# Kernel optimization log

Measured on AMD Instinct MI355X. Metric: run time of the kernel, lower is better.

## Reference

```python
import jax, jax.numpy as jnp
import numpy as np

B, N, M = 16, 2048, 2048


def setup_inputs() -> dict:
    key = jax.random.key(0)
    k1, k2, k3 = jax.random.split(key, 3)
    pred_dsmat = jax.random.uniform(k1, (B, N, M), dtype=jnp.float32)
    # valid sizes: src_ns <= tgt_ns so a permutation GT exists for every valid row
    src_ns = jax.random.randint(k2, (B,), 1024, 1537, dtype=jnp.int32)
    tgt_ns = jax.random.randint(k3, (B,), 1537, 2049, dtype=jnp.int32)
    # gt_perm: identity permutation restricted to the valid region (one 1 per valid row)
    i = jnp.arange(N)[:, None]
    j = jnp.arange(M)[None, :]
    eye = (i == j).astype(jnp.float32)  # [N, M]
    row_mask = (jnp.arange(N)[None, :] < src_ns[:, None]).astype(jnp.float32)  # [B, N]
    gt_perm = eye[None, :, :] * row_mask[:, :, None]  # [B, N, M]
    return {"pred_dsmat": pred_dsmat, "gt_perm": gt_perm,
            "src_ns": src_ns, "tgt_ns": tgt_ns, "beta_value": 0.1}


def reference(pred_dsmat, gt_perm, src_ns, tgt_ns, beta_value):
    Bn, Nn, Mn = pred_dsmat.shape
    row_mask = jnp.arange(Nn)[None, :] < src_ns[:, None]   # [B, N] bool
    col_mask = jnp.arange(Mn)[None, :] < tgt_ns[:, None]   # [B, M] bool
    mask = row_mask[:, :, None] & col_mask[:, None, :]     # [B, N, M]

    pred = jnp.clip(pred_dsmat, 0.0, 1.0) * mask
    gt = gt_perm * mask

    gt_pred = pred * gt                      # gt-selected predicted values
    row_gt = gt_pred.sum(axis=2)             # [B, N] per-row GT value
    col_gt = gt_pred.sum(axis=1)             # [B, M] per-col GT value
    row_cnt = gt.sum(axis=2)                 # [B, N] #GT matches per row
    col_cnt = gt.sum(axis=1)                 # [B, M] #GT matches per col

    # attention masks: entries >= (gt value - beta), restricted to valid region
    att_src = ((pred >= row_gt[:, :, None] - beta_value) & mask) * row_cnt[:, :, None]
    att_tgt = ((pred >= col_gt[:, None, :] - beta_value) & mask) * col_cnt[:, None, :]

    src_neg = jnp.sum(((att_src - gt) * pred) ** 2, axis=2)  # [B, N]
    src_pos = jnp.sum(gt_pred ** 2, axis=2)                  # [B, N]
    tgt_neg = jnp.sum(((att_tgt - gt) * pred) ** 2, axis=1)  # [B, M]

    # sum of tgt_neg over the GT-matched column of each row == dot with column counts
    corr = jnp.einsum('bm,bm->b', tgt_neg, col_cnt)          # [B]

    denom = 1.0 + src_neg + corr[:, None]                    # [B, N]
    num = jnp.where(row_mask, src_pos, 1.0)
    den = jnp.where(row_mask, denom, 1.0)
    loss = -0.5 * jnp.sum(jnp.log(num / den) * row_mask)
    n_sum = src_ns.sum().astype(pred.dtype)
    return loss / n_sum
```

## Files before the change

### kernel.cpp

```cpp
#include <hip/hip_runtime.h>

#define B_ 16
#define N_ 2048
#define M_ 2048
#define ROWS 64
#define WROWS 16

__device__ __forceinline__ float wave_sum(float v) {
#pragma unroll
    for (int off = 32; off >= 1; off >>= 1) v += __shfl_xor(v, off);
    return v;
}

extern "C" __global__ __launch_bounds__(256) void k_pass1(
    const float* __restrict__ pred, const float* __restrict__ gt,
    const int* __restrict__ src_ns, const int* __restrict__ tgt_ns,
    float* __restrict__ row_gt, float* __restrict__ row_cnt,
    float* __restrict__ col_gt, float* __restrict__ col_cnt)
{
    const int b = blockIdx.y;
    const int src = src_ns[b];
    const int band = blockIdx.x;
    if (band * ROWS >= src) return;
    const int tgt = tgt_ns[b];
    const int wave = threadIdx.x >> 6, lane = threadIdx.x & 63;
    const int base = b * (N_ * M_);

    float4 acg[8], accn[8];
#pragma unroll
    for (int j = 0; j < 8; ++j) { acg[j] = make_float4(0,0,0,0); accn[j] = make_float4(0,0,0,0); }

    const int row0 = band * ROWS + wave * WROWS;
    for (int r = 0; r < WROWS; ++r) {
        const int n = row0 + r;
        if (n >= src) break;
        const float4* prow = (const float4*)(pred + base + n * M_);
        const float4* grow = (const float4*)(gt + base + n * M_);
        float rg = 0.f, rc = 0.f;
#pragma unroll
        for (int j = 0; j < 8; ++j) {
            const int m4 = j * 64 + lane;
            const float4 p4 = prow[m4];
            const float4 g4 = grow[m4];
            const int mb = m4 * 4;
#define P1C(K, MB) do { \
    const bool ok = (mb + K) < tgt; \
    float p = fminf(fmaxf(p4.MB, 0.f), 1.f); p = ok ? p : 0.f; \
    const float g = ok ? g4.MB : 0.f; \
    const float gp = p * g; \
    rg += gp; rc += g; \
    acg[j].MB += gp; accn[j].MB += g; \
} while (0)
            P1C(0, x); P1C(1, y); P1C(2, z); P1C(3, w);
#undef P1C
        }
        rg = wave_sum(rg); rc = wave_sum(rc);
        if (lane == 0) { row_gt[b * N_ + n] = rg; row_cnt[b * N_ + n] = rc; }
    }

    __shared__ float4 s_cg[M_ / 4];
    __shared__ float4 s_cc[M_ / 4];
    for (int i = threadIdx.x; i < M_ / 4; i += 256) {
        s_cg[i] = make_float4(0,0,0,0);
        s_cc[i] = make_float4(0,0,0,0);
    }
    __syncthreads();
    for (int w = 0; w < 4; ++w) {
        if (wave == w) {
#pragma unroll
            for (int j = 0; j < 8; ++j) {
                const int i = j * 64 + lane;
                float4 v = s_cg[i];
                v.x += acg[j].x; v.y += acg[j].y; v.z += acg[j].z; v.w += acg[j].w;
                s_cg[i] = v;
                float4 u = s_cc[i];
                u.x += accn[j].x; u.y += accn[j].y; u.z += accn[j].z; u.w += accn[j].w;
                s_cc[i] = u;
            }
        }
        __syncthreads();
    }
    const float* fcg = (const float*)s_cg;
    const float* fcc = (const float*)s_cc;
    for (int i = threadIdx.x; i < M_; i += 256) {
        atomicAdd(&col_gt[b * M_ + i], fcg[i]);
        atomicAdd(&col_cnt[b * M_ + i], fcc[i]);
    }
}

extern "C" __global__ __launch_bounds__(256) void k_pass2(
    const float* __restrict__ pred, const float* __restrict__ gt,
    const int* __restrict__ src_ns, const int* __restrict__ tgt_ns,
    const float* __restrict__ beta_p,
    const float* __restrict__ row_gt, const float* __restrict__ row_cnt,
    const float* __restrict__ col_gt, const float* __restrict__ col_cnt,
    float* __restrict__ src_neg, float* __restrict__ src_pos,
    float* __restrict__ tgt_neg)
{
    const int b = blockIdx.y;
    const int src = src_ns[b];
    const int band = blockIdx.x;
    if (band * ROWS >= src) return;
    const int tgt = tgt_ns[b];
    const float beta = beta_p[0];
    const int wave = threadIdx.x >> 6, lane = threadIdx.x & 63;
    const int base = b * (N_ * M_);

    float4 cg[8], cc[8], tn[8];
    const float4* cg4 = (const float4*)(col_gt + b * M_);
    const float4* cc4 = (const float4*)(col_cnt + b * M_);
#pragma unroll
    for (int j = 0; j < 8; ++j) {
        cg[j] = cg4[j * 64 + lane];
        cc[j] = cc4[j * 64 + lane];
        tn[j] = make_float4(0,0,0,0);
    }

    const int row0 = band * ROWS + wave * WROWS;
    for (int r = 0; r < WROWS; ++r) {
        const int n = row0 + r;
        if (n >= src) break;
        const float rg = row_gt[b * N_ + n];
        const float rc = row_cnt[b * N_ + n];
        const float rth = rg - beta;
        const float4* prow = (const float4*)(pred + base + n * M_);
        const float4* grow = (const float4*)(gt + base + n * M_);
        float sneg = 0.f, spos = 0.f;
#pragma unroll
        for (int j = 0; j < 8; ++j) {
            const int m4 = j * 64 + lane;
            const float4 p4 = prow[m4];
            const float4 g4 = grow[m4];
            const int mb = m4 * 4;
#define P2C(K, MB) do { \
    const bool ok = (mb + K) < tgt; \
    float p = fminf(fmaxf(p4.MB, 0.f), 1.f); p = ok ? p : 0.f; \
    const float g = ok ? g4.MB : 0.f; \
    const float gp = p * g; \
    const float as = (ok && (p >= rth)) ? rc : 0.f; \
    const float ds = (as - g) * p; \
    sneg += ds * ds; spos += gp * gp; \
    const float at = (ok && (p >= cg[j].MB - beta)) ? cc[j].MB : 0.f; \
    const float dt = (at - g) * p; \
    tn[j].MB += dt * dt; \
} while (0)
            P2C(0, x); P2C(1, y); P2C(2, z); P2C(3, w);
#undef P2C
        }
        sneg = wave_sum(sneg); spos = wave_sum(spos);
        if (lane == 0) { src_neg[b * N_ + n] = sneg; src_pos[b * N_ + n] = spos; }
    }

    __shared__ float4 s_tn[M_ / 4];
    for (int i = threadIdx.x; i < M_ / 4; i += 256) s_tn[i] = make_float4(0,0,0,0);
    __syncthreads();
    for (int w = 0; w < 4; ++w) {
        if (wave == w) {
#pragma unroll
            for (int j = 0; j < 8; ++j) {
                const int i = j * 64 + lane;
                float4 v = s_tn[i];
                v.x += tn[j].x; v.y += tn[j].y; v.z += tn[j].z; v.w += tn[j].w;
                s_tn[i] = v;
            }
        }
        __syncthreads();
    }
    const float* ftn = (const float*)s_tn;
    for (int i = threadIdx.x; i < M_; i += 256)
        atomicAdd(&tgt_neg[b * M_ + i], ftn[i]);
}

extern "C" __global__ __launch_bounds__(256) void k_final(
    const float* __restrict__ src_neg, const float* __restrict__ src_pos,
    const float* __restrict__ tgt_neg, const float* __restrict__ col_cnt,
    const int* __restrict__ src_ns, float* __restrict__ out)
{
    const int b = blockIdx.x;
    const int wave = threadIdx.x >> 6, lane = threadIdx.x & 63;
    __shared__ float sredc[4];
    __shared__ float sredl[4];

    float c = 0.f;
    for (int i = threadIdx.x; i < M_; i += 256)
        c += tgt_neg[b * M_ + i] * col_cnt[b * M_ + i];
    c = wave_sum(c);
    if (lane == 0) sredc[wave] = c;
    __syncthreads();
    const float corr = sredc[0] + sredc[1] + sredc[2] + sredc[3];

    const int src = src_ns[b];
    float ls = 0.f;
    for (int n = threadIdx.x; n < src; n += 256) {
        const float sp = src_pos[b * N_ + n];
        const float sn = src_neg[b * N_ + n];
        ls += logf(sp) - logf(1.f + sn + corr);
    }
    ls = wave_sum(ls);
    if (lane == 0) sredl[wave] = ls;
    __syncthreads();
    if (threadIdx.x == 0) {
        const float total = sredl[0] + sredl[1] + sredl[2] + sredl[3];
        float nsum = 0.f;
        for (int i = 0; i < B_; ++i) nsum += (float)src_ns[i];
        atomicAdd(out, -0.5f * total / nsum);
    }
}

extern "C" void kernel_launch(void* const* d_in, const int* in_sizes, int n_in,
                              void* d_out, int out_size, void* d_ws, size_t ws_size,
                              hipStream_t stream)
{
    const float* pred   = (const float*)d_in[0];
    const float* gtp    = (const float*)d_in[1];
    const int*   src_ns = (const int*)d_in[2];
    const int*   tgt_ns = (const int*)d_in[3];
    const float* beta   = (const float*)d_in[4];
    float* out = (float*)d_out;
    float* ws  = (float*)d_ws;

    float* row_gt  = ws;
    float* row_cnt = row_gt  + B_ * N_;
    float* col_gt  = row_cnt + B_ * N_;
    float* col_cnt = col_gt  + B_ * M_;
    float* src_neg = col_cnt + B_ * M_;
    float* src_pos = src_neg + B_ * N_;
    float* tgt_neg = src_pos + B_ * N_;

    const size_t zero_bytes = (size_t)(4 * B_ * N_ + 3 * B_ * M_) * sizeof(float);
    hipMemsetAsync(d_ws, 0, zero_bytes, stream);
    hipMemsetAsync(d_out, 0, sizeof(float), stream);

    dim3 grid(N_ / ROWS, B_);
    k_pass1<<<grid, 256, 0, stream>>>(pred, gtp, src_ns, tgt_ns,
                                      row_gt, row_cnt, col_gt, col_cnt);
    k_pass2<<<grid, 256, 0, stream>>>(pred, gtp, src_ns, tgt_ns, beta,
                                      row_gt, row_cnt, col_gt, col_cnt,
                                      src_neg, src_pos, tgt_neg);
    k_final<<<B_, 256, 0, stream>>>(src_neg, src_pos, tgt_neg, col_cnt, src_ns, out);
}
```

Baseline: 565.6 us.

## Split batch into groups for L2/LLC reuse, skip invalid column chunks and zero atomics

Passes 1 and 2 now run over groups of 8 batches, so pass 2 re-reads pred/gt while the group's data may still sit in the large last-level cache. The band size is halved to raise block count. Column chunks past tgt_ns are skipped, zero-valued atomics are suppressed, and the memset is shrunk to only the atomically accumulated buffers. This adds two extra kernel launches and relies on each group's working set fitting in cache.

```diff
diff --git a/kernel.cpp b/kernel.cpp
--- a/kernel.cpp
+++ b/kernel.cpp
@@ -3,8 +3,9 @@
 #define B_ 16
 #define N_ 2048
 #define M_ 2048
-#define ROWS 64
-#define WROWS 16
+#define ROWS 32
+#define WROWS 8
+#define GRP 8
 
 __device__ __forceinline__ float wave_sum(float v) {
 #pragma unroll
@@ -16,9 +17,9 @@
     const float* __restrict__ pred, const float* __restrict__ gt,
     const int* __restrict__ src_ns, const int* __restrict__ tgt_ns,
     float* __restrict__ row_gt, float* __restrict__ row_cnt,
-    float* __restrict__ col_gt, float* __restrict__ col_cnt)
-{
-    const int b = blockIdx.y;
+    float* __restrict__ col_gt, float* __restrict__ col_cnt, int b0)
+{
+    const int b = b0 + blockIdx.y;
     const int src = src_ns[b];
     const int band = blockIdx.x;
     if (band * ROWS >= src) return;
@@ -39,6 +40,7 @@
         float rg = 0.f, rc = 0.f;
 #pragma unroll
         for (int j = 0; j < 8; ++j) {
+            if (j * 256 >= tgt) break;
             const int m4 = j * 64 + lane;
             const float4 p4 = prow[m4];
             const float4 g4 = grow[m4];
@@ -83,8 +85,10 @@
     const float* fcg = (const float*)s_cg;
     const float* fcc = (const float*)s_cc;
     for (int i = threadIdx.x; i < M_; i += 256) {
-        atomicAdd(&col_gt[b * M_ + i], fcg[i]);
-        atomicAdd(&col_cnt[b * M_ + i], fcc[i]);
+        const float v = fcg[i];
+        const float u = fcc[i];
+        if (v != 0.f) atomicAdd(&col_gt[b * M_ + i], v);
+        if (u != 0.f) atomicAdd(&col_cnt[b * M_ + i], u);
     }
 }
 
@@ -95,9 +99,9 @@
     const float* __restrict__ row_gt, const float* __restrict__ row_cnt,
     const float* __restrict__ col_gt, const float* __restrict__ col_cnt,
     float* __restrict__ src_neg, float* __restrict__ src_pos,
-    float* __restrict__ tgt_neg)
-{
-    const int b = blockIdx.y;
+    float* __restrict__ tgt_neg, int b0)
+{
+    const int b = b0 + blockIdx.y;
     const int src = src_ns[b];
     const int band = blockIdx.x;
     if (band * ROWS >= src) return;
@@ -111,9 +115,14 @@
     const float4* cc4 = (const float4*)(col_cnt + b * M_);
 #pragma unroll
     for (int j = 0; j < 8; ++j) {
-        cg[j] = cg4[j * 64 + lane];
-        cc[j] = cc4[j * 64 + lane];
         tn[j] = make_float4(0,0,0,0);
+        if (j * 256 < tgt) {
+            cg[j] = cg4[j * 64 + lane];
+            cc[j] = cc4[j * 64 + lane];
+        } else {
+            cg[j] = make_float4(0,0,0,0);
+            cc[j] = make_float4(0,0,0,0);
+        }
     }
 
     const int row0 = band * ROWS + wave * WROWS;
@@ -128,6 +137,7 @@
         float sneg = 0.f, spos = 0.f;
 #pragma unroll
         for (int j = 0; j < 8; ++j) {
+            if (j * 256 >= tgt) break;
             const int m4 = j * 64 + lane;
             const float4 p4 = prow[m4];
             const float4 g4 = grow[m4];
@@ -167,8 +177,10 @@
         __syncthreads();
     }
     const float* ftn = (const float*)s_tn;
-    for (int i = threadIdx.x; i < M_; i += 256)
-        atomicAdd(&tgt_neg[b * M_ + i], ftn[i]);
+    for (int i = threadIdx.x; i < M_; i += 256) {
+        const float v = ftn[i];
+        if (v != 0.f) atomicAdd(&tgt_neg[b * M_ + i], v);
+    }
 }
 
 extern "C" __global__ __launch_bounds__(256) void k_final(
@@ -219,23 +231,26 @@
     float* out = (float*)d_out;
     float* ws  = (float*)d_ws;
 
-    float* row_gt  = ws;
+    float* col_gt  = ws;
+    float* col_cnt = col_gt  + B_ * M_;
+    float* tgt_neg = col_cnt + B_ * M_;
+    float* row_gt  = tgt_neg + B_ * M_;
     float* row_cnt = row_gt  + B_ * N_;
-    float* col_gt  = row_cnt + B_ * N_;
-    float* col_cnt = col_gt  + B_ * M_;
-    float* src_neg = col_cnt + B_ * M_;
+    float* src_neg = row_cnt + B_ * N_;
     float* src_pos = src_neg + B_ * N_;
-    float* tgt_neg = src_pos + B_ * N_;
-
-    const size_t zero_bytes = (size_t)(4 * B_ * N_ + 3 * B_ * M_) * sizeof(float);
+
+    const size_t zero_bytes = (size_t)(3 * B_ * M_) * sizeof(float);
     hipMemsetAsync(d_ws, 0, zero_bytes, stream);
     hipMemsetAsync(d_out, 0, sizeof(float), stream);
 
-    dim3 grid(N_ / ROWS, B_);
-    k_pass1<<<grid, 256, 0, stream>>>(pred, gtp, src_ns, tgt_ns,
-                                      row_gt, row_cnt, col_gt, col_cnt);
-    k_pass2<<<grid, 256, 0, stream>>>(pred, gtp, src_ns, tgt_ns, beta,
-                                      row_gt, row_cnt, col_gt, col_cnt,
-                                      src_neg, src_pos, tgt_neg);
+    dim3 grid(N_ / ROWS, GRP);
+    for (int g = 0; g < B_ / GRP; ++g) {
+        const int b0 = g * GRP;
+        k_pass1<<<grid, 256, 0, stream>>>(pred, gtp, src_ns, tgt_ns,
+                                          row_gt, row_cnt, col_gt, col_cnt, b0);
+        k_pass2<<<grid, 256, 0, stream>>>(pred, gtp, src_ns, tgt_ns, beta,
+                                          row_gt, row_cnt, col_gt, col_cnt,
+                                          src_neg, src_pos, tgt_neg, b0);
+    }
     k_final<<<B_, 256, 0, stream>>>(src_neg, src_pos, tgt_neg, col_cnt, src_ns, out);
 }
```

New measurement: 598.1 us. +5.7%, slower.

## Exploit gt sparsity: scan gt once, stream pred only, correct sparse terms

Applied to the files above, without the earlier changes.

Splits the work into a pass that reads only gt and records its nonzero entries (at most two per row) with atomics, a dense pass that streams only pred using an expanded formula that drops the gt terms, and a final pass that adds the sparse gt correction terms. This removes the second full read of gt and the dense pred read in pass one, cutting total memory traffic from four full tensor reads to two. It also halves the rows per block and skips column chunks beyond tgt. The correction assumes at most two nonzeros per gt row, which holds for permutation inputs but is not general, and it adds contended atomics and extra workspace.

```diff
diff --git a/kernel.cpp b/kernel.cpp
--- a/kernel.cpp
+++ b/kernel.cpp
@@ -3,8 +3,10 @@
 #define B_ 16
 #define N_ 2048
 #define M_ 2048
-#define ROWS 64
-#define WROWS 16
+#define ROWS 32
+#define WROWS 8
+#define BN (B_ * N_)
+#define BM (B_ * M_)
 
 __device__ __forceinline__ float wave_sum(float v) {
 #pragma unroll
@@ -12,147 +14,124 @@
     return v;
 }
 
-extern "C" __global__ __launch_bounds__(256) void k_pass1(
-    const float* __restrict__ pred, const float* __restrict__ gt,
+extern "C" __global__ __launch_bounds__(256) void k_scan_gt(
+    const float* __restrict__ gt, const float* __restrict__ pred,
     const int* __restrict__ src_ns, const int* __restrict__ tgt_ns,
     float* __restrict__ row_gt, float* __restrict__ row_cnt,
-    float* __restrict__ col_gt, float* __restrict__ col_cnt)
+    float* __restrict__ col_gt, float* __restrict__ col_cnt,
+    int* __restrict__ sp_cnt, int* __restrict__ sp_m,
+    float* __restrict__ sp_g, float* __restrict__ sp_p)
 {
     const int b = blockIdx.y;
     const int src = src_ns[b];
-    const int band = blockIdx.x;
-    if (band * ROWS >= src) return;
+    if (blockIdx.x * ROWS >= src) return;
     const int tgt = tgt_ns[b];
     const int wave = threadIdx.x >> 6, lane = threadIdx.x & 63;
     const int base = b * (N_ * M_);
-
-    float4 acg[8], accn[8];
-#pragma unroll
-    for (int j = 0; j < 8; ++j) { acg[j] = make_float4(0,0,0,0); accn[j] = make_float4(0,0,0,0); }
-
-    const int row0 = band * ROWS + wave * WROWS;
+    const int row0 = blockIdx.x * ROWS + wave * WROWS;
+
     for (int r = 0; r < WROWS; ++r) {
         const int n = row0 + r;
         if (n >= src) break;
-        const float4* prow = (const float4*)(pred + base + n * M_);
         const float4* grow = (const float4*)(gt + base + n * M_);
-        float rg = 0.f, rc = 0.f;
 #pragma unroll
         for (int j = 0; j < 8; ++j) {
+            if (j * 256 >= tgt) break;
             const int m4 = j * 64 + lane;
-            const float4 p4 = prow[m4];
             const float4 g4 = grow[m4];
             const int mb = m4 * 4;
-#define P1C(K, MB) do { \
-    const bool ok = (mb + K) < tgt; \
-    float p = fminf(fmaxf(p4.MB, 0.f), 1.f); p = ok ? p : 0.f; \
-    const float g = ok ? g4.MB : 0.f; \
-    const float gp = p * g; \
-    rg += gp; rc += g; \
-    acg[j].MB += gp; accn[j].MB += g; \
+#define SCAN(K, MB) do { \
+    const int m = mb + K; \
+    const float gv = g4.MB; \
+    if (m < tgt && gv != 0.f) { \
+        float pv = pred[base + n * M_ + m]; \
+        pv = fminf(fmaxf(pv, 0.f), 1.f); \
+        const int bn = b * N_ + n; \
+        const float gp = pv * gv; \
+        atomicAdd(&row_gt[bn], gp); \
+        atomicAdd(&row_cnt[bn], gv); \
+        atomicAdd(&col_gt[b * M_ + m], gp); \
+        atomicAdd(&col_cnt[b * M_ + m], gv); \
+        const int slot = atomicAdd(&sp_cnt[bn], 1); \
+        if (slot < 2) { \
+            sp_m[slot * BN + bn] = m; \
+            sp_g[slot * BN + bn] = gv; \
+            sp_p[slot * BN + bn] = pv; \
+        } \
+    } \
 } while (0)
-            P1C(0, x); P1C(1, y); P1C(2, z); P1C(3, w);
-#undef P1C
-        }
-        rg = wave_sum(rg); rc = wave_sum(rc);
-        if (lane == 0) { row_gt[b * N_ + n] = rg; row_cnt[b * N_ + n] = rc; }
-    }
-
-    __shared__ float4 s_cg[M_ / 4];
-    __shared__ float4 s_cc[M_ / 4];
-    for (int i = threadIdx.x; i < M_ / 4; i += 256) {
-        s_cg[i] = make_float4(0,0,0,0);
-        s_cc[i] = make_float4(0,0,0,0);
-    }
-    __syncthreads();
-    for (int w = 0; w < 4; ++w) {
-        if (wave == w) {
-#pragma unroll
-            for (int j = 0; j < 8; ++j) {
-                const int i = j * 64 + lane;
-                float4 v = s_cg[i];
-                v.x += acg[j].x; v.y += acg[j].y; v.z += acg[j].z; v.w += acg[j].w;
-                s_cg[i] = v;
-                float4 u = s_cc[i];
-                u.x += accn[j].x; u.y += accn[j].y; u.z += accn[j].z; u.w += accn[j].w;
-                s_cc[i] = u;
-            }
-        }
-        __syncthreads();
-    }
-    const float* fcg = (const float*)s_cg;
-    const float* fcc = (const float*)s_cc;
-    for (int i = threadIdx.x; i < M_; i += 256) {
-        atomicAdd(&col_gt[b * M_ + i], fcg[i]);
-        atomicAdd(&col_cnt[b * M_ + i], fcc[i]);
-    }
-}
-
-extern "C" __global__ __launch_bounds__(256) void k_pass2(
-    const float* __restrict__ pred, const float* __restrict__ gt,
+            SCAN(0, x); SCAN(1, y); SCAN(2, z); SCAN(3, w);
+#undef SCAN
+        }
+    }
+}
+
+extern "C" __global__ __launch_bounds__(256) void k_stream_pred(
+    const float* __restrict__ pred,
     const int* __restrict__ src_ns, const int* __restrict__ tgt_ns,
     const float* __restrict__ beta_p,
     const float* __restrict__ row_gt, const float* __restrict__ row_cnt,
     const float* __restrict__ col_gt, const float* __restrict__ col_cnt,
-    float* __restrict__ src_neg, float* __restrict__ src_pos,
-    float* __restrict__ tgt_neg)
+    float* __restrict__ src_neg, float* __restrict__ tgt_neg)
 {
     const int b = blockIdx.y;
     const int src = src_ns[b];
-    const int band = blockIdx.x;
-    if (band * ROWS >= src) return;
+    if (blockIdx.x * ROWS >= src) return;
     const int tgt = tgt_ns[b];
     const float beta = beta_p[0];
     const int wave = threadIdx.x >> 6, lane = threadIdx.x & 63;
     const int base = b * (N_ * M_);
 
-    float4 cg[8], cc[8], tn[8];
+    float4 cgb[8], cc2[8], tn[8];
     const float4* cg4 = (const float4*)(col_gt + b * M_);
     const float4* cc4 = (const float4*)(col_cnt + b * M_);
 #pragma unroll
     for (int j = 0; j < 8; ++j) {
-        cg[j] = cg4[j * 64 + lane];
-        cc[j] = cc4[j * 64 + lane];
-        tn[j] = make_float4(0,0,0,0);
-    }
-
-    const int row0 = band * ROWS + wave * WROWS;
+        tn[j] = make_float4(0, 0, 0, 0);
+        if (j * 256 < tgt) {
+            const float4 cg = cg4[j * 64 + lane];
+            const float4 cv = cc4[j * 64 + lane];
+            cgb[j] = make_float4(cg.x - beta, cg.y - beta, cg.z - beta, cg.w - beta);
+            cc2[j] = make_float4(cv.x * cv.x, cv.y * cv.y, cv.z * cv.z, cv.w * cv.w);
+        } else {
+            cgb[j] = make_float4(0, 0, 0, 0);
+            cc2[j] = make_float4(0, 0, 0, 0);
+        }
+    }
+
+    const int row0 = blockIdx.x * ROWS + wave * WROWS;
     for (int r = 0; r < WROWS; ++r) {
         const int n = row0 + r;
         if (n >= src) break;
-        const float rg = row_gt[b * N_ + n];
-        const float rc = row_cnt[b * N_ + n];
+        const int bn = b * N_ + n;
+        const float rg = row_gt[bn];
+        const float rc = row_cnt[bn];
         const float rth = rg - beta;
+        const float rc2 = rc * rc;
         const float4* prow = (const float4*)(pred + base + n * M_);
-        const float4* grow = (const float4*)(gt + base + n * M_);
-        float sneg = 0.f, spos = 0.f;
+        float sneg = 0.f;
 #pragma unroll
         for (int j = 0; j < 8; ++j) {
+            if (j * 256 >= tgt) break;
             const int m4 = j * 64 + lane;
             const float4 p4 = prow[m4];
-            const float4 g4 = grow[m4];
             const int mb = m4 * 4;
-#define P2C(K, MB) do { \
+#define DENSE(K, MB) do { \
     const bool ok = (mb + K) < tgt; \
     float p = fminf(fmaxf(p4.MB, 0.f), 1.f); p = ok ? p : 0.f; \
-    const float g = ok ? g4.MB : 0.f; \
-    const float gp = p * g; \
-    const float as = (ok && (p >= rth)) ? rc : 0.f; \
-    const float ds = (as - g) * p; \
-    sneg += ds * ds; spos += gp * gp; \
-    const float at = (ok && (p >= cg[j].MB - beta)) ? cc[j].MB : 0.f; \
-    const float dt = (at - g) * p; \
-    tn[j].MB += dt * dt; \
+    const float ps = p * p; \
+    sneg += (p >= rth) ? rc2 * ps : 0.f; \
+    tn[j].MB += (p >= cgb[j].MB) ? cc2[j].MB * ps : 0.f; \
 } while (0)
-            P2C(0, x); P2C(1, y); P2C(2, z); P2C(3, w);
-#undef P2C
-        }
-        sneg = wave_sum(sneg); spos = wave_sum(spos);
-        if (lane == 0) { src_neg[b * N_ + n] = sneg; src_pos[b * N_ + n] = spos; }
+            DENSE(0, x); DENSE(1, y); DENSE(2, z); DENSE(3, w);
+#undef DENSE
+        }
+        sneg = wave_sum(sneg);
+        if (lane == 0) src_neg[bn] = sneg;
     }
 
     __shared__ float4 s_tn[M_ / 4];
-    for (int i = threadIdx.x; i < M_ / 4; i += 256) s_tn[i] = make_float4(0,0,0,0);
+    for (int i = threadIdx.x; i < M_ / 4; i += 256) s_tn[i] = make_float4(0, 0, 0, 0);
     __syncthreads();
     for (int w = 0; w < 4; ++w) {
         if (wave == w) {
@@ -167,19 +146,52 @@
         __syncthreads();
     }
     const float* ftn = (const float*)s_tn;
-    for (int i = threadIdx.x; i < M_; i += 256)
-        atomicAdd(&tgt_neg[b * M_ + i], ftn[i]);
+    for (int i = threadIdx.x; i < M_; i += 256) {
+        const float v = ftn[i];
+        if (v != 0.f) atomicAdd(&tgt_neg[b * M_ + i], v);
+    }
 }
 
 extern "C" __global__ __launch_bounds__(256) void k_final(
-    const float* __restrict__ src_neg, const float* __restrict__ src_pos,
-    const float* __restrict__ tgt_neg, const float* __restrict__ col_cnt,
-    const int* __restrict__ src_ns, float* __restrict__ out)
+    const int* __restrict__ src_ns, const float* __restrict__ beta_p,
+    const float* __restrict__ row_gt, const float* __restrict__ row_cnt,
+    const float* __restrict__ col_gt, const float* __restrict__ col_cnt,
+    const int* __restrict__ sp_cnt, const int* __restrict__ sp_m,
+    const float* __restrict__ sp_g, const float* __restrict__ sp_p,
+    float* __restrict__ src_neg, float* __restrict__ src_pos,
+    float* __restrict__ tgt_neg, float* __restrict__ out)
 {
     const int b = blockIdx.x;
+    const float beta = beta_p[0];
     const int wave = threadIdx.x >> 6, lane = threadIdx.x & 63;
     __shared__ float sredc[4];
     __shared__ float sredl[4];
+
+    for (int n = threadIdx.x; n < N_; n += 256) {
+        const int bn = b * N_ + n;
+        int cnt = sp_cnt[bn];
+        if (cnt <= 0) continue;
+        if (cnt > 2) cnt = 2;
+        const float rg = row_gt[bn];
+        const float rc = row_cnt[bn];
+        float add_pos = 0.f, add_neg = 0.f;
+        for (int s = 0; s < cnt; ++s) {
+            const int m = sp_m[s * BN + bn];
+            const float gv = sp_g[s * BN + bn];
+            const float pv = sp_p[s * BN + bn];
+            const float pv2 = pv * pv;
+            add_pos += (pv * gv) * (pv * gv);
+            const float as = (pv >= rg - beta) ? rc : 0.f;
+            add_neg += (gv * gv - 2.f * as * gv) * pv2;
+            const float ccm = col_cnt[b * M_ + m];
+            const float at = (pv >= col_gt[b * M_ + m] - beta) ? ccm : 0.f;
+            atomicAdd(&tgt_neg[b * M_ + m], (gv * gv - 2.f * at * gv) * pv2);
+        }
+        src_pos[bn] += add_pos;
+        src_neg[bn] += add_neg;
+    }
+    __threadfence();
+    __syncthreads();
 
     float c = 0.f;
     for (int i = threadIdx.x; i < M_; i += 256)
@@ -219,23 +231,30 @@
     float* out = (float*)d_out;
     float* ws  = (float*)d_ws;
 
-    float* row_gt  = ws;
-    float* row_cnt = row_gt  + B_ * N_;
-    float* col_gt  = row_cnt + B_ * N_;
-    float* col_cnt = col_gt  + B_ * M_;
-    float* src_neg = col_cnt + B_ * M_;
-    float* src_pos = src_neg + B_ * N_;
-    float* tgt_neg = src_pos + B_ * N_;
-
-    const size_t zero_bytes = (size_t)(4 * B_ * N_ + 3 * B_ * M_) * sizeof(float);
+    float* col_gt  = ws;
+    float* col_cnt = col_gt  + BM;
+    float* tgt_neg = col_cnt + BM;
+    float* row_gt  = tgt_neg + BM;
+    float* row_cnt = row_gt  + BN;
+    float* src_pos = row_cnt + BN;
+    int*   sp_cnt  = (int*)(src_pos + BN);
+    float* src_neg = (float*)(sp_cnt + BN);
+    int*   sp_m    = (int*)(src_neg + BN);
+    float* sp_g    = (float*)(sp_m + 2 * BN);
+    float* sp_p    = sp_g + 2 * BN;
+
+    const size_t zero_bytes = (size_t)(3 * BM + 4 * BN) * sizeof(float);
     hipMemsetAsync(d_ws, 0, zero_bytes, stream);
     hipMemsetAsync(d_out, 0, sizeof(float), stream);
 
     dim3 grid(N_ / ROWS, B_);
-    k_pass1<<<grid, 256, 0, stream>>>(pred, gtp, src_ns, tgt_ns,
-                                      row_gt, row_cnt, col_gt, col_cnt);
-    k_pass2<<<grid, 256, 0, stream>>>(pred, gtp, src_ns, tgt_ns, beta,
-                                      row_gt, row_cnt, col_gt, col_cnt,
-                                      src_neg, src_pos, tgt_neg);
-    k_final<<<B_, 256, 0, stream>>>(src_neg, src_pos, tgt_neg, col_cnt, src_ns, out);
-}
+    k_scan_gt<<<grid, 256, 0, stream>>>(gtp, pred, src_ns, tgt_ns,
+                                        row_gt, row_cnt, col_gt, col_cnt,
+                                        sp_cnt, sp_m, sp_g, sp_p);
+    k_stream_pred<<<grid, 256, 0, stream>>>(pred, src_ns, tgt_ns, beta,
+                                            row_gt, row_cnt, col_gt, col_cnt,
+                                            src_neg, tgt_neg);
+    k_final<<<B_, 256, 0, stream>>>(src_ns, beta, row_gt, row_cnt,
+                                    col_gt, col_cnt, sp_cnt, sp_m, sp_g, sp_p,
+                                    src_neg, src_pos, tgt_neg, out);
+}
```

Result: no change. 566.9 us (+0.2%).
